# Kernel optimization log

Measured on AMD Instinct MI355X. Metric: run time of the kernel, lower is better.

## Reference

```python
import jax, jax.numpy as jnp
import numpy as np

B, S, D = 4, 2048, 1024
H = 4096          # adapter hidden dim
E = 4             # number of adapters / experts


def setup_inputs() -> dict:
    key = jax.random.key(0)
    ks = jax.random.split(key, 7)
    sd = 1.0 / np.sqrt(D)
    sh = 1.0 / np.sqrt(H)
    return {
        "x":  jax.random.normal(ks[0], (B, S, D), dtype=jnp.float32),
        "Wr": jax.random.uniform(ks[1], (D, E), minval=-sd, maxval=sd, dtype=jnp.float32),
        "br": jax.random.uniform(ks[2], (E,), minval=-sd, maxval=sd, dtype=jnp.float32),
        "W1": jax.random.uniform(ks[3], (E, D, H), minval=-sd, maxval=sd, dtype=jnp.float32),
        "b1": jax.random.uniform(ks[4], (E, H), minval=-sd, maxval=sd, dtype=jnp.float32),
        "W2": jax.random.uniform(ks[5], (E, H, D), minval=-sh, maxval=sh, dtype=jnp.float32),
        "b2": jax.random.uniform(ks[6], (E, D), minval=-sh, maxval=sh, dtype=jnp.float32),
    }


def reference(x, Wr, br, W1, b1, W2, b2):
    # Flatten tokens: (N, D)
    xf = x.reshape(-1, D)
    N = xf.shape[0]

    # Top-1 router (route_type='none' -> router input is x itself)
    logits = xf @ Wr + br                      # (N, E)
    probs = jax.nn.softmax(logits, axis=-1)    # (N, E)
    gate_idx = jnp.argmax(probs, axis=-1)      # (N,) int
    gate_val = jnp.max(probs, axis=-1)         # (N,)

    # Run every expert adapter densely (E small), then select per token.
    h = jnp.einsum('nd,edh->enh', xf, W1) + b1[:, None, :]   # (E, N, H)
    h = jax.nn.silu(h)
    eo = jnp.einsum('enh,ehd->end', h, W2) + b2[:, None, :]  # (E, N, D)

    sel = eo[gate_idx, jnp.arange(N)]          # (N, D) per-token expert output
    out = sel * gate_val[:, None]              # is_scale_prob=True scaling
    return out.reshape(B, S, D)
```

## Files before the change

### kernel.cpp

```cpp
#include <hip/hip_runtime.h>

#define DN 8192
#define DD 1024
#define DH 4096
#define DE 4
#define SLOTS (DN + DE * 256)
#define RT (SLOTS / 256)

typedef unsigned short u16;
typedef float f32x4 __attribute__((ext_vector_type(4)));
typedef __bf16 bf16x8 __attribute__((ext_vector_type(8)));
typedef u16 u16x2 __attribute__((ext_vector_type(2)));
typedef u16 u16x4 __attribute__((ext_vector_type(4)));

__device__ __forceinline__ u16 f2b(float f) {
  union { float f; unsigned u; } v; v.f = f;
  return (u16)((v.u + 0x7FFFu + ((v.u >> 16) & 1u)) >> 16);
}

__device__ __forceinline__ void gl_lds16(const u16* g, u16* l) {
  __builtin_amdgcn_global_load_lds((const __attribute__((address_space(1))) void*)g,
                                   (__attribute__((address_space(3))) void*)l, 16, 0, 0);
}

__global__ __launch_bounds__(256) void router_k(const float* __restrict__ x,
    const float* __restrict__ Wr, const float* __restrict__ br,
    float* __restrict__ gval, int* __restrict__ gidx, int* __restrict__ gpos,
    int* __restrict__ counts, u16* __restrict__ xb)
{
  const int tid = blockIdx.x * 256 + threadIdx.x;
  const int n = tid >> 6, lane = tid & 63;
  const float* xr = x + (size_t)n * DD;
  double a0 = 0., a1 = 0., a2 = 0., a3 = 0.;
#pragma unroll
  for (int k = 0; k < DD / 64; ++k) {
    const int d = lane + k * 64;
    const float xv = xr[d];
    const f32x4 w = *(const f32x4*)&Wr[d * 4];
    a0 += (double)xv * w[0]; a1 += (double)xv * w[1];
    a2 += (double)xv * w[2]; a3 += (double)xv * w[3];
    xb[(size_t)n * DD + d] = f2b(xv);
  }
#pragma unroll
  for (int off = 32; off; off >>= 1) {
    a0 += __shfl_xor(a0, off);
    a1 += __shfl_xor(a1, off);
    a2 += __shfl_xor(a2, off);
    a3 += __shfl_xor(a3, off);
  }
  if (lane == 0) {
    const double l0 = a0 + br[0], l1 = a1 + br[1], l2 = a2 + br[2], l3 = a3 + br[3];
    int bi = 0; double bm = l0;
    if (l1 > bm) { bm = l1; bi = 1; }
    if (l2 > bm) { bm = l2; bi = 2; }
    if (l3 > bm) { bm = l3; bi = 3; }
    const float s = __expf((float)(l0 - bm)) + __expf((float)(l1 - bm)) +
                    __expf((float)(l2 - bm)) + __expf((float)(l3 - bm));
    gval[n] = 1.0f / s;
    gidx[n] = bi;
    gpos[n] = atomicAdd(&counts[bi], 1);
  }
}

__global__ void offsets_k(const int* __restrict__ counts, int* __restrict__ offs) {
  if (threadIdx.x == 0 && blockIdx.x == 0) {
    int o = 0;
#pragma unroll
    for (int e = 0; e < DE; ++e) { offs[e] = o; o += (counts[e] + 255) & ~255; }
    offs[DE] = o;
  }
}

__global__ __launch_bounds__(256) void scatter_k(const int* __restrict__ gidx,
    const int* __restrict__ gpos, const int* __restrict__ offs, int* __restrict__ tlist) {
  const int n = blockIdx.x * 256 + threadIdx.x;
  tlist[offs[gidx[n]] + gpos[n]] = n;
}

__global__ __launch_bounds__(256) void transpose_conv(const float* __restrict__ in,
    u16* __restrict__ out, int R, int C)
{
  __shared__ u16 t[64][66];
  const int r0 = blockIdx.x * 64, c0 = blockIdx.y * 64;
  const size_t mo = (size_t)blockIdx.z * R * C;
  const int tid = threadIdx.x;
  const int i = tid >> 4, j0 = (tid & 15) * 4;
#pragma unroll
  for (int k = 0; k < 4; ++k) {
    const int row = k * 16 + i;
    const f32x4 v = *(const f32x4*)&in[mo + (size_t)(r0 + row) * C + c0 + j0];
    u16x2 u01; u01[0] = f2b(v[0]); u01[1] = f2b(v[1]);
    u16x2 u23; u23[0] = f2b(v[2]); u23[1] = f2b(v[3]);
    *(u16x2*)&t[row][j0] = u01;
    *(u16x2*)&t[row][j0 + 2] = u23;
  }
  __syncthreads();
#pragma unroll
  for (int k = 0; k < 4; ++k) {
    const int p = k * 16 + i;
    u16x4 u;
    u[0] = t[j0 + 0][p]; u[1] = t[j0 + 1][p]; u[2] = t[j0 + 2][p]; u[3] = t[j0 + 3][p];
    *(u16x4*)&out[mo + (size_t)(c0 + p) * R + r0 + j0] = u;
  }
}

#define STAGE(t, B) do { \
    gl_lds16(pa0 + (size_t)(t) * 32, &As[B][kc][rb0][0]); \
    gl_lds16(pa1 + (size_t)(t) * 32, &As[B][kc][rb0 + 64][0]); \
    gl_lds16(pb0 + (size_t)(t) * 32, &Bs[B][kc][rb0][0]); \
    gl_lds16(pb1 + (size_t)(t) * 32, &Bs[B][kc][rb0 + 64][0]); \
  } while (0)

#define COMPUTE(B) do { \
    bf16x8 af[8], bfv[4]; \
    _Pragma("unroll") \
    for (int m = 0; m < 8; ++m) af[m] = *(const bf16x8*)&As[B][fq][wr + m * 16 + fr][0]; \
    _Pragma("unroll") \
    for (int n = 0; n < 4; ++n) bfv[n] = *(const bf16x8*)&Bs[B][fq][wc + n * 16 + fr][0]; \
    __builtin_amdgcn_s_setprio(1); \
    _Pragma("unroll") \
    for (int m = 0; m < 8; ++m) \
      _Pragma("unroll") \
      for (int n = 0; n < 4; ++n) \
        acc[m][n] = __builtin_amdgcn_mfma_f32_16x16x32_bf16(af[m], bfv[n], acc[m][n], 0, 0, 0); \
    __builtin_amdgcn_s_setprio(0); \
  } while (0)

#define GI(t, CUR, NXT) do { \
    STAGE((t) + 1, NXT); \
    COMPUTE(CUR); \
    __builtin_amdgcn_sched_barrier(0); \
    asm volatile("s_waitcnt vmcnt(0)" ::: "memory"); \
    __builtin_amdgcn_s_barrier(); \
    __builtin_amdgcn_sched_barrier(0); \
  } while (0)

__global__ __launch_bounds__(512, 2) void gemm1_k(const u16* __restrict__ xb,
    const u16* __restrict__ w1t, const float* __restrict__ b1,
    const int* __restrict__ tlist, const int* __restrict__ offs, u16* __restrict__ hb)
{
  __shared__ u16 As[2][4][256][8];
  __shared__ u16 Bs[2][4][256][8];
  const int nwg = RT * (DH / 256);
  const int bq = nwg >> 3;
  const int wg = (blockIdx.x & 7) * bq + (blockIdx.x >> 3);
  const int row0 = (wg % RT) * 256;
  const int h0 = (wg / RT) * 256;
  if (row0 >= offs[DE]) return;
  int e = 0;
  if (row0 >= offs[1]) e = 1;
  if (row0 >= offs[2]) e = 2;
  if (row0 >= offs[3]) e = 3;
  const int tid = threadIdx.x;
  const int wid = tid >> 6, lane = tid & 63;
  const int kc = wid >> 1, rb0 = (wid & 1) * 128;

  int tA0 = tlist[row0 + rb0 + lane];
  int tA1 = tlist[row0 + rb0 + 64 + lane];
  if (tA0 < 0) tA0 = 0;
  if (tA1 < 0) tA1 = 0;
  const u16* pa0 = xb + (size_t)tA0 * DD + kc * 8;
  const u16* pa1 = xb + (size_t)tA1 * DD + kc * 8;
  const u16* pb0 = w1t + ((size_t)e * DH + h0 + rb0 + lane) * DD + kc * 8;
  const u16* pb1 = pb0 + (size_t)64 * DD;

  const int wr = (wid >> 2) * 128, wc = (wid & 3) * 64;
  const int fr = lane & 15, fq = lane >> 4;

  f32x4 acc[8][4];
#pragma unroll
  for (int m = 0; m < 8; ++m)
#pragma unroll
    for (int n = 0; n < 4; ++n) acc[m][n] = (f32x4)(0.f);

  STAGE(0, 0);
  asm volatile("s_waitcnt vmcnt(0)" ::: "memory");
  __builtin_amdgcn_s_barrier();
  __builtin_amdgcn_sched_barrier(0);
#define NK1 (DD / 32)
#pragma unroll 1
  for (int ks = 0; ks < NK1 - 2; ks += 2) {
    GI(ks, 0, 1);
    GI(ks + 1, 1, 0);
  }
  GI(NK1 - 2, 0, 1);
  COMPUTE(1);

#pragma unroll
  for (int n = 0; n < 4; ++n) {
    const int h = h0 + wc + n * 16 + fr;
    const float bias = b1[(size_t)e * DH + h];
#pragma unroll
    for (int m = 0; m < 8; ++m) {
      const int r = row0 + wr + m * 16 + fq * 4;
      const f32x4 v = acc[m][n];
#pragma unroll
      for (int i = 0; i < 4; ++i) {
        const float xv = v[i] + bias;
        const float sv = xv / (1.f + __expf(-xv));
        hb[(size_t)(r + i) * DH + h] = f2b(sv);
      }
    }
  }
}

__global__ __launch_bounds__(512, 2) void gemm2_k(const u16* __restrict__ hb,
    const u16* __restrict__ w2t, const int* __restrict__ tlist,
    const int* __restrict__ offs, float* __restrict__ out, float* __restrict__ p1)
{
  __shared__ u16 As[2][4][256][8];
  __shared__ u16 Bs[2][4][256][8];
  const int nwg = RT * (DD / 256) * 2;
  const int bq = nwg >> 3;
  const int wg = (blockIdx.x & 7) * bq + (blockIdx.x >> 3);
  const int row0 = (wg % RT) * 256;
  const int rest = wg / RT;
  const int d0 = (rest & 3) * 256;
  const int kb = (rest >> 2) * (DH / 2);
  if (row0 >= offs[DE]) return;
  int e = 0;
  if (row0 >= offs[1]) e = 1;
  if (row0 >= offs[2]) e = 2;
  if (row0 >= offs[3]) e = 3;
  const int tid = threadIdx.x;
  const int wid = tid >> 6, lane = tid & 63;
  const int kc = wid >> 1, rb0 = (wid & 1) * 128;

  const u16* pa0 = hb + ((size_t)(row0 + rb0 + lane)) * DH + kb + kc * 8;
  const u16* pa1 = pa0 + (size_t)64 * DH;
  const u16* pb0 = w2t + ((size_t)e * DD + d0 + rb0 + lane) * DH + kb + kc * 8;
  const u16* pb1 = pb0 + (size_t)64 * DH;

  const int wr = (wid >> 2) * 128, wc = (wid & 3) * 64;
  const int fr = lane & 15, fq = lane >> 4;

  f32x4 acc[8][4];
#pragma unroll
  for (int m = 0; m < 8; ++m)
#pragma unroll
    for (int n = 0; n < 4; ++n) acc[m][n] = (f32x4)(0.f);

  STAGE(0, 0);
  asm volatile("s_waitcnt vmcnt(0)" ::: "memory");
  __builtin_amdgcn_s_barrier();
  __builtin_amdgcn_sched_barrier(0);
#define NK2 (DH / 2 / 32)
#pragma unroll 1
  for (int ks = 0; ks < NK2 - 2; ks += 2) {
    GI(ks, 0, 1);
    GI(ks + 1, 1, 0);
  }
  GI(NK2 - 2, 0, 1);
  COMPUTE(1);

  float* __restrict__ dst = (kb == 0) ? out : p1;
  int tok[8][4];
#pragma unroll
  for (int m = 0; m < 8; ++m) {
    const int rb = row0 + wr + m * 16 + fq * 4;
#pragma unroll
    for (int i = 0; i < 4; ++i) tok[m][i] = tlist[rb + i];
  }
#pragma unroll
  for (int n = 0; n < 4; ++n) {
    const int d = d0 + wc + n * 16 + fr;
#pragma unroll
    for (int m = 0; m < 8; ++m)
#pragma unroll
      for (int i = 0; i < 4; ++i) {
        const int t = tok[m][i];
        if (t >= 0) dst[(size_t)t * DD + d] = acc[m][n][i];
      }
  }
}

__global__ __launch_bounds__(256) void reduce2_k(float* __restrict__ out,
    const float* __restrict__ p1, const float* __restrict__ b2,
    const int* __restrict__ gidx, const float* __restrict__ gval)
{
  const size_t idx = ((size_t)blockIdx.x * 256 + threadIdx.x) * 4;
  const int n = (int)(idx >> 10);
  const int d = (int)(idx & (DD - 1));
  const int e = gidx[n];
  const float g = gval[n];
  f32x4 a = *(f32x4*)&out[idx];
  const f32x4 b = *(const f32x4*)&p1[idx];
  const f32x4 bb = *(const f32x4*)&b2[(size_t)e * DD + d];
  f32x4 r;
#pragma unroll
  for (int j = 0; j < 4; ++j) r[j] = (a[j] + b[j] + bb[j]) * g;
  *(f32x4*)&out[idx] = r;
}

extern "C" void kernel_launch(void* const* d_in, const int* in_sizes, int n_in,
                              void* d_out, int out_size, void* d_ws, size_t ws_size,
                              hipStream_t stream) {
  const float* x  = (const float*)d_in[0];
  const float* Wr = (const float*)d_in[1];
  const float* br = (const float*)d_in[2];
  const float* W1 = (const float*)d_in[3];
  const float* b1 = (const float*)d_in[4];
  const float* W2 = (const float*)d_in[5];
  const float* b2 = (const float*)d_in[6];
  float* out = (float*)d_out;

  char* ws = (char*)d_ws;
  int*   counts = (int*)ws;
  int*   offs   = (int*)(ws + 256);
  float* gval   = (float*)(ws + 512);
  int*   gidx   = (int*)(ws + 512 + 32768);
  int*   gpos   = (int*)(ws + 512 + 65536);
  int*   tlist  = (int*)(ws + 512 + 98304);
  size_t off = 512 + 98304 + 36864;
  u16* xb  = (u16*)(ws + off);
  float* p1 = (float*)(ws + off);
  off += (size_t)DN * DD * 2;
  u16* w1t = (u16*)(ws + off); off += (size_t)DE * DH * DD * 2;
  u16* w2t = (u16*)(ws + off); off += (size_t)DE * DD * DH * 2;
  u16* hb  = (u16*)(ws + off);

  hipMemsetAsync(counts, 0, 256, stream);
  hipMemsetAsync(tlist, 0xFF, SLOTS * sizeof(int), stream);

  router_k<<<dim3(DN / 4), 256, 0, stream>>>(x, Wr, br, gval, gidx, gpos, counts, xb);
  offsets_k<<<dim3(1), 64, 0, stream>>>(counts, offs);
  scatter_k<<<dim3(DN / 256), 256, 0, stream>>>(gidx, gpos, offs, tlist);
  transpose_conv<<<dim3(DD / 64, DH / 64, DE), 256, 0, stream>>>(W1, w1t, DD, DH);
  transpose_conv<<<dim3(DH / 64, DD / 64, DE), 256, 0, stream>>>(W2, w2t, DH, DD);
  gemm1_k<<<dim3(RT * (DH / 256)), 512, 0, stream>>>(xb, w1t, b1, tlist, offs, hb);
  gemm2_k<<<dim3(RT * (DD / 256) * 2), 512, 0, stream>>>(hb, w2t, tlist, offs, out, p1);
  reduce2_k<<<dim3(DN * DD / 4 / 256), 256, 0, stream>>>(out, p1, b2, gidx, gval);
}
```

Measured before the change: 703.5 us.

## Deepen GEMM pipeline to 64-wide K tiles, drop split-K and reduce kernel

Both grouped GEMMs now stage 64-wide K tiles as two 32-wide halves and interleave loads with half-width MFMA phases, waiting with vmcnt(4) instead of draining all loads each step. gemm2 no longer splits K in two; it adds the bias and gate scaling in its epilogue, which removes the partial buffer and the separate reduce kernel. The two weight transpose/convert launches are merged into one. The catch is half as many gemm2 workgroups, which lowers occupancy and parallelism across CUs, plus doubled LDS per block with more barriers.

```diff
diff --git a/kernel.cpp b/kernel.cpp
--- a/kernel.cpp
+++ b/kernel.cpp
@@ -77,12 +77,24 @@
   tlist[offs[gidx[n]] + gpos[n]] = n;
 }
 
-__global__ __launch_bounds__(256) void transpose_conv(const float* __restrict__ in,
-    u16* __restrict__ out, int R, int C)
+__global__ __launch_bounds__(256) void transpose_all(const float* __restrict__ W1,
+    const float* __restrict__ W2, u16* __restrict__ w1t, u16* __restrict__ w2t)
 {
   __shared__ u16 t[64][66];
-  const int r0 = blockIdx.x * 64, c0 = blockIdx.y * 64;
-  const size_t mo = (size_t)blockIdx.z * R * C;
+  const int id = blockIdx.x;
+  const float* in; u16* out; int R, C, r0, c0; size_t mo;
+  if (id < 4096) {
+    const int e = id >> 10, tt = id & 1023;
+    in = W1; out = w1t; R = DD; C = DH;
+    r0 = (tt >> 6) * 64; c0 = (tt & 63) * 64;
+    mo = (size_t)e * DD * DH;
+  } else {
+    const int t2 = id - 4096;
+    const int e = t2 >> 10, tt = t2 & 1023;
+    in = W2; out = w2t; R = DH; C = DD;
+    r0 = (tt >> 4) * 64; c0 = (tt & 15) * 64;
+    mo = (size_t)e * DD * DH;
+  }
   const int tid = threadIdx.x;
   const int i = tid >> 4, j0 = (tid & 15) * 4;
 #pragma unroll
@@ -104,46 +116,44 @@
   }
 }
 
-#define STAGE(t, B) do { \
-    gl_lds16(pa0 + (size_t)(t) * 32, &As[B][kc][rb0][0]); \
-    gl_lds16(pa1 + (size_t)(t) * 32, &As[B][kc][rb0 + 64][0]); \
-    gl_lds16(pb0 + (size_t)(t) * 32, &Bs[B][kc][rb0][0]); \
-    gl_lds16(pb1 + (size_t)(t) * 32, &Bs[B][kc][rb0 + 64][0]); \
-  } while (0)
-
-#define COMPUTE(B) do { \
-    bf16x8 af[8], bfv[4]; \
-    _Pragma("unroll") \
-    for (int m = 0; m < 8; ++m) af[m] = *(const bf16x8*)&As[B][fq][wr + m * 16 + fr][0]; \
-    _Pragma("unroll") \
-    for (int n = 0; n < 4; ++n) bfv[n] = *(const bf16x8*)&Bs[B][fq][wc + n * 16 + fr][0]; \
+
+#define PH(C_, KS_, NH_, STG, WAITC) do { \
+    if ((NH_) == 0) { \
+      _Pragma("unroll") \
+      for (int m = 0; m < 8; ++m) \
+        af[m] = *(const bf16x8*)&As[C_][KS_][fq][wr + m * 16 + fr][0]; \
+    } \
+    bf16x8 bf0 = *(const bf16x8*)&Bs[C_][KS_][fq][wc + ((NH_)*2) * 16 + fr][0]; \
+    bf16x8 bf1 = *(const bf16x8*)&Bs[C_][KS_][fq][wc + ((NH_)*2 + 1) * 16 + fr][0]; \
+    STG; \
+    __builtin_amdgcn_s_barrier(); \
+    asm volatile("s_waitcnt lgkmcnt(0)" ::: "memory"); \
+    __builtin_amdgcn_sched_barrier(0); \
     __builtin_amdgcn_s_setprio(1); \
     _Pragma("unroll") \
-    for (int m = 0; m < 8; ++m) \
-      _Pragma("unroll") \
-      for (int n = 0; n < 4; ++n) \
-        acc[m][n] = __builtin_amdgcn_mfma_f32_16x16x32_bf16(af[m], bfv[n], acc[m][n], 0, 0, 0); \
+    for (int m = 0; m < 8; ++m) { \
+      acc[m][(NH_)*2]     = __builtin_amdgcn_mfma_f32_16x16x32_bf16(af[m], bf0, acc[m][(NH_)*2], 0, 0, 0); \
+      acc[m][(NH_)*2 + 1] = __builtin_amdgcn_mfma_f32_16x16x32_bf16(af[m], bf1, acc[m][(NH_)*2 + 1], 0, 0, 0); \
+    } \
     __builtin_amdgcn_s_setprio(0); \
-  } while (0)
-
-#define GI(t, CUR, NXT) do { \
-    STAGE((t) + 1, NXT); \
-    COMPUTE(CUR); \
     __builtin_amdgcn_sched_barrier(0); \
-    asm volatile("s_waitcnt vmcnt(0)" ::: "memory"); \
+    WAITC; \
     __builtin_amdgcn_s_barrier(); \
     __builtin_amdgcn_sched_barrier(0); \
   } while (0)
+
+#define VM4 asm volatile("s_waitcnt vmcnt(4)" ::: "memory")
+#define VM0 asm volatile("s_waitcnt vmcnt(0)" ::: "memory")
 
 __global__ __launch_bounds__(512, 2) void gemm1_k(const u16* __restrict__ xb,
     const u16* __restrict__ w1t, const float* __restrict__ b1,
     const int* __restrict__ tlist, const int* __restrict__ offs, u16* __restrict__ hb)
 {
-  __shared__ u16 As[2][4][256][8];
-  __shared__ u16 Bs[2][4][256][8];
+  __shared__ u16 As[2][2][4][256][8];
+  __shared__ u16 Bs[2][2][4][256][8];
   const int nwg = RT * (DH / 256);
   const int bq = nwg >> 3;
-  const int wg = (blockIdx.x & 7) * bq + (blockIdx.x >> 3);
+  const int wg = ((int)blockIdx.x & 7) * bq + ((int)blockIdx.x >> 3);
   const int row0 = (wg % RT) * 256;
   const int h0 = (wg / RT) * 256;
   if (row0 >= offs[DE]) return;
@@ -153,16 +163,23 @@
   if (row0 >= offs[3]) e = 3;
   const int tid = threadIdx.x;
   const int wid = tid >> 6, lane = tid & 63;
-  const int kc = wid >> 1, rb0 = (wid & 1) * 128;
-
-  int tA0 = tlist[row0 + rb0 + lane];
-  int tA1 = tlist[row0 + rb0 + 64 + lane];
-  if (tA0 < 0) tA0 = 0;
-  if (tA1 < 0) tA1 = 0;
-  const u16* pa0 = xb + (size_t)tA0 * DD + kc * 8;
-  const u16* pa1 = xb + (size_t)tA1 * DD + kc * 8;
-  const u16* pb0 = w1t + ((size_t)e * DH + h0 + rb0 + lane) * DD + kc * 8;
-  const u16* pb1 = pb0 + (size_t)64 * DD;
+  const int kcs = wid & 3;
+  const int ra0 = ((wid >> 2) * 2) * 64;
+  const int ra1 = ra0 + 64;
+
+  int tokA0 = tlist[row0 + ra0 + lane]; if (tokA0 < 0) tokA0 = 0;
+  int tokA1 = tlist[row0 + ra1 + lane]; if (tokA1 < 0) tokA1 = 0;
+  const u16* paA0 = xb + (size_t)tokA0 * DD + kcs * 8;
+  const u16* paA1 = xb + (size_t)tokA1 * DD + kcs * 8;
+  const u16* pbB0 = w1t + ((size_t)e * DH + h0 + ra0 + lane) * DD + kcs * 8;
+  const u16* pbB1 = pbB0 + (size_t)64 * DD;
+
+#define SA(t, h, c) do { \
+    gl_lds16(paA0 + (t) * 64 + (h) * 32, &As[c][h][kcs][ra0][0]); \
+    gl_lds16(paA1 + (t) * 64 + (h) * 32, &As[c][h][kcs][ra1][0]); } while (0)
+#define SB(t, h, c) do { \
+    gl_lds16(pbB0 + (size_t)(t) * 64 + (h) * 32, &Bs[c][h][kcs][ra0][0]); \
+    gl_lds16(pbB1 + (size_t)(t) * 64 + (h) * 32, &Bs[c][h][kcs][ra1][0]); } while (0)
 
   const int wr = (wid >> 2) * 128, wc = (wid & 3) * 64;
   const int fr = lane & 15, fq = lane >> 4;
@@ -172,19 +189,31 @@
   for (int m = 0; m < 8; ++m)
 #pragma unroll
     for (int n = 0; n < 4; ++n) acc[m][n] = (f32x4)(0.f);
-
-  STAGE(0, 0);
-  asm volatile("s_waitcnt vmcnt(0)" ::: "memory");
+  bf16x8 af[8];
+
+  SA(0, 0, 0); SB(0, 0, 0); SA(0, 1, 0); SB(0, 1, 0);
+  VM4;
   __builtin_amdgcn_s_barrier();
   __builtin_amdgcn_sched_barrier(0);
-#define NK1 (DD / 32)
+
+#define NT1 (DD / 64)
 #pragma unroll 1
-  for (int ks = 0; ks < NK1 - 2; ks += 2) {
-    GI(ks, 0, 1);
-    GI(ks + 1, 1, 0);
-  }
-  GI(NK1 - 2, 0, 1);
-  COMPUTE(1);
+  for (int tt = 0; tt < NT1 - 1; ++tt) {
+    const int c = tt & 1, nc = c ^ 1;
+    PH(c, 0, 0, SA(tt + 1, 0, nc), );
+    PH(c, 0, 1, SB(tt + 1, 0, nc), VM4);
+    PH(c, 1, 0, SA(tt + 1, 1, nc), );
+    PH(c, 1, 1, SB(tt + 1, 1, nc), VM4);
+  }
+  {
+    const int c = (NT1 - 1) & 1;
+    PH(c, 0, 0, , );
+    PH(c, 0, 1, , VM0);
+    PH(c, 1, 0, , );
+    PH(c, 1, 1, , );
+  }
+#undef SA
+#undef SB
 
 #pragma unroll
   for (int n = 0; n < 4; ++n) {
@@ -205,18 +234,17 @@
 }
 
 __global__ __launch_bounds__(512, 2) void gemm2_k(const u16* __restrict__ hb,
-    const u16* __restrict__ w2t, const int* __restrict__ tlist,
-    const int* __restrict__ offs, float* __restrict__ out, float* __restrict__ p1)
+    const u16* __restrict__ w2t, const float* __restrict__ b2,
+    const int* __restrict__ tlist, const int* __restrict__ offs,
+    const float* __restrict__ gval, float* __restrict__ out)
 {
-  __shared__ u16 As[2][4][256][8];
-  __shared__ u16 Bs[2][4][256][8];
-  const int nwg = RT * (DD / 256) * 2;
+  __shared__ u16 As[2][2][4][256][8];
+  __shared__ u16 Bs[2][2][4][256][8];
+  const int nwg = RT * (DD / 256);
   const int bq = nwg >> 3;
-  const int wg = (blockIdx.x & 7) * bq + (blockIdx.x >> 3);
+  const int wg = ((int)blockIdx.x & 7) * bq + ((int)blockIdx.x >> 3);
   const int row0 = (wg % RT) * 256;
-  const int rest = wg / RT;
-  const int d0 = (rest & 3) * 256;
-  const int kb = (rest >> 2) * (DH / 2);
+  const int d0 = (wg / RT) * 256;
   if (row0 >= offs[DE]) return;
   int e = 0;
   if (row0 >= offs[1]) e = 1;
@@ -224,12 +252,21 @@
   if (row0 >= offs[3]) e = 3;
   const int tid = threadIdx.x;
   const int wid = tid >> 6, lane = tid & 63;
-  const int kc = wid >> 1, rb0 = (wid & 1) * 128;
-
-  const u16* pa0 = hb + ((size_t)(row0 + rb0 + lane)) * DH + kb + kc * 8;
-  const u16* pa1 = pa0 + (size_t)64 * DH;
-  const u16* pb0 = w2t + ((size_t)e * DD + d0 + rb0 + lane) * DH + kb + kc * 8;
-  const u16* pb1 = pb0 + (size_t)64 * DH;
+  const int kcs = wid & 3;
+  const int ra0 = ((wid >> 2) * 2) * 64;
+  const int ra1 = ra0 + 64;
+
+  const u16* paA0 = hb + (size_t)(row0 + ra0 + lane) * DH + kcs * 8;
+  const u16* paA1 = paA0 + (size_t)64 * DH;
+  const u16* pbB0 = w2t + ((size_t)e * DD + d0 + ra0 + lane) * DH + kcs * 8;
+  const u16* pbB1 = pbB0 + (size_t)64 * DH;
+
+#define SA(t, h, c) do { \
+    gl_lds16(paA0 + (size_t)(t) * 64 + (h) * 32, &As[c][h][kcs][ra0][0]); \
+    gl_lds16(paA1 + (size_t)(t) * 64 + (h) * 32, &As[c][h][kcs][ra1][0]); } while (0)
+#define SB(t, h, c) do { \
+    gl_lds16(pbB0 + (size_t)(t) * 64 + (h) * 32, &Bs[c][h][kcs][ra0][0]); \
+    gl_lds16(pbB1 + (size_t)(t) * 64 + (h) * 32, &Bs[c][h][kcs][ra1][0]); } while (0)
 
   const int wr = (wid >> 2) * 128, wc = (wid & 3) * 64;
   const int fr = lane & 15, fq = lane >> 4;
@@ -239,57 +276,55 @@
   for (int m = 0; m < 8; ++m)
 #pragma unroll
     for (int n = 0; n < 4; ++n) acc[m][n] = (f32x4)(0.f);
-
-  STAGE(0, 0);
-  asm volatile("s_waitcnt vmcnt(0)" ::: "memory");
+  bf16x8 af[8];
+
+  SA(0, 0, 0); SB(0, 0, 0); SA(0, 1, 0); SB(0, 1, 0);
+  VM4;
   __builtin_amdgcn_s_barrier();
   __builtin_amdgcn_sched_barrier(0);
-#define NK2 (DH / 2 / 32)
+
+#define NT2 (DH / 64)
 #pragma unroll 1
-  for (int ks = 0; ks < NK2 - 2; ks += 2) {
-    GI(ks, 0, 1);
-    GI(ks + 1, 1, 0);
-  }
-  GI(NK2 - 2, 0, 1);
-  COMPUTE(1);
-
-  float* __restrict__ dst = (kb == 0) ? out : p1;
-  int tok[8][4];
+  for (int tt = 0; tt < NT2 - 1; ++tt) {
+    const int c = tt & 1, nc = c ^ 1;
+    PH(c, 0, 0, SA(tt + 1, 0, nc), );
+    PH(c, 0, 1, SB(tt + 1, 0, nc), VM4);
+    PH(c, 1, 0, SA(tt + 1, 1, nc), );
+    PH(c, 1, 1, SB(tt + 1, 1, nc), VM4);
+  }
+  {
+    const int c = (NT2 - 1) & 1;
+    PH(c, 0, 0, , );
+    PH(c, 0, 1, , VM0);
+    PH(c, 1, 0, , );
+    PH(c, 1, 1, , );
+  }
+#undef SA
+#undef SB
+
+  int tok[8][4]; float gv[8][4];
 #pragma unroll
   for (int m = 0; m < 8; ++m) {
     const int rb = row0 + wr + m * 16 + fq * 4;
 #pragma unroll
-    for (int i = 0; i < 4; ++i) tok[m][i] = tlist[rb + i];
+    for (int i = 0; i < 4; ++i) {
+      const int t = tlist[rb + i];
+      tok[m][i] = t;
+      gv[m][i] = (t >= 0) ? gval[t] : 0.f;
+    }
   }
 #pragma unroll
   for (int n = 0; n < 4; ++n) {
     const int d = d0 + wc + n * 16 + fr;
+    const float bias = b2[(size_t)e * DD + d];
 #pragma unroll
     for (int m = 0; m < 8; ++m)
 #pragma unroll
       for (int i = 0; i < 4; ++i) {
         const int t = tok[m][i];
-        if (t >= 0) dst[(size_t)t * DD + d] = acc[m][n][i];
+        if (t >= 0) out[(size_t)t * DD + d] = (acc[m][n][i] + bias) * gv[m][i];
       }
   }
-}
-
-__global__ __launch_bounds__(256) void reduce2_k(float* __restrict__ out,
-    const float* __restrict__ p1, const float* __restrict__ b2,
-    const int* __restrict__ gidx, const float* __restrict__ gval)
-{
-  const size_t idx = ((size_t)blockIdx.x * 256 + threadIdx.x) * 4;
-  const int n = (int)(idx >> 10);
-  const int d = (int)(idx & (DD - 1));
-  const int e = gidx[n];
-  const float g = gval[n];
-  f32x4 a = *(f32x4*)&out[idx];
-  const f32x4 b = *(const f32x4*)&p1[idx];
-  const f32x4 bb = *(const f32x4*)&b2[(size_t)e * DD + d];
-  f32x4 r;
-#pragma unroll
-  for (int j = 0; j < 4; ++j) r[j] = (a[j] + b[j] + bb[j]) * g;
-  *(f32x4*)&out[idx] = r;
 }
 
 extern "C" void kernel_launch(void* const* d_in, const int* in_sizes, int n_in,
@@ -312,9 +347,7 @@
   int*   gpos   = (int*)(ws + 512 + 65536);
   int*   tlist  = (int*)(ws + 512 + 98304);
   size_t off = 512 + 98304 + 36864;
-  u16* xb  = (u16*)(ws + off);
-  float* p1 = (float*)(ws + off);
-  off += (size_t)DN * DD * 2;
+  u16* xb  = (u16*)(ws + off); off += (size_t)DN * DD * 2;
   u16* w1t = (u16*)(ws + off); off += (size_t)DE * DH * DD * 2;
   u16* w2t = (u16*)(ws + off); off += (size_t)DE * DD * DH * 2;
   u16* hb  = (u16*)(ws + off);
@@ -325,9 +358,7 @@
   router_k<<<dim3(DN / 4), 256, 0, stream>>>(x, Wr, br, gval, gidx, gpos, counts, xb);
   offsets_k<<<dim3(1), 64, 0, stream>>>(counts, offs);
   scatter_k<<<dim3(DN / 256), 256, 0, stream>>>(gidx, gpos, offs, tlist);
-  transpose_conv<<<dim3(DD / 64, DH / 64, DE), 256, 0, stream>>>(W1, w1t, DD, DH);
-  transpose_conv<<<dim3(DH / 64, DD / 64, DE), 256, 0, stream>>>(W2, w2t, DH, DD);
+  transpose_all<<<dim3(8192), 256, 0, stream>>>(W1, W2, w1t, w2t);
   gemm1_k<<<dim3(RT * (DH / 256)), 512, 0, stream>>>(xb, w1t, b1, tlist, offs, hb);
-  gemm2_k<<<dim3(RT * (DD / 256) * 2), 512, 0, stream>>>(hb, w2t, tlist, offs, out, p1);
-  reduce2_k<<<dim3(DN * DD / 4 / 256), 256, 0, stream>>>(out, p1, b2, gidx, gval);
-}
+  gemm2_k<<<dim3(RT * (DD / 256)), 512, 0, stream>>>(hb, w2t, b2, tlist, offs, gval, out);
+}
```

Measured after the change: 631.6 us. -10.2%, faster.
